# Kernel tuning notes

Hardware: AMD Instinct MI355X
Metric: run time of the kernel (lower is better)

The kernel has to match this reference:

```python
import jax, jax.numpy as jnp
import numpy as np

D = 512      # d_model
H = 8        # n_heads
DH = D // H  # d_head
WIN = 128    # window radius
FF = 4 * D   # ffn hidden
B, T = 4, 2048
EPS = 1e-5


def _ln(x, g, b):
    mu = jnp.mean(x, axis=-1, keepdims=True)
    var = jnp.mean((x - mu) ** 2, axis=-1, keepdims=True)
    return (x - mu) * jax.lax.rsqrt(var + EPS) * g + b


def _rope(x):
    # standard rotate-half RoPE over the full d_model dim (applied to ln(x)
    # before q/k/v projections, as in the source module)
    t, d = x.shape[-2], x.shape[-1]
    half = d // 2
    inv_freq = 1.0 / (10000.0 ** (jnp.arange(half, dtype=jnp.float32) / half))
    ang = jnp.arange(t, dtype=jnp.float32)[:, None] * inv_freq[None, :]  # (T, half)
    cos, sin = jnp.cos(ang), jnp.sin(ang)
    x1, x2 = x[..., :half], x[..., half:]
    return jnp.concatenate([x1 * cos - x2 * sin, x1 * sin + x2 * cos], axis=-1)


def setup_inputs() -> dict:
    key = jax.random.key(0)
    ks = jax.random.split(key, 16)
    s = 0.02
    inp = {
        "x": jax.random.normal(ks[0], (B, T, D), dtype=jnp.float32),
        "Wq": jax.random.normal(ks[1], (D, D), dtype=jnp.float32) * s,
        "bq": jnp.zeros((D,), jnp.float32),
        "Wk": jax.random.normal(ks[2], (D, D), dtype=jnp.float32) * s,
        "bk": jnp.zeros((D,), jnp.float32),
        "Wv": jax.random.normal(ks[3], (D, D), dtype=jnp.float32) * s,
        "bv": jnp.zeros((D,), jnp.float32),
        "Wo": jax.random.normal(ks[4], (D, D), dtype=jnp.float32) * s,
        "bo": jnp.zeros((D,), jnp.float32),
        "ln_g": jnp.ones((D,), jnp.float32),
        "ln_b": jnp.zeros((D,), jnp.float32),
        "ffln_g": jnp.ones((D,), jnp.float32),
        "ffln_b": jnp.zeros((D,), jnp.float32),
        "W1": jax.random.normal(ks[5], (D, FF), dtype=jnp.float32) * s,
        "b1": jnp.zeros((FF,), jnp.float32),
        "W2": jax.random.normal(ks[6], (FF, D), dtype=jnp.float32) * s,
        "b2": jnp.zeros((D,), jnp.float32),
    }
    return inp


def reference(x, Wq, bq, Wk, bk, Wv, bv, Wo, bo, ln_g, ln_b, ffln_g, ffln_b, W1, b1, W2, b2):
    b, t, d = x.shape
    h = _rope(_ln(x, ln_g, ln_b))
    q = (h @ Wq + bq).reshape(b, t, H, DH).transpose(0, 2, 1, 3)  # (B,H,T,DH)
    k = (h @ Wk + bk).reshape(b, t, H, DH).transpose(0, 2, 1, 3)
    v = (h @ Wv + bv).reshape(b, t, H, DH).transpose(0, 2, 1, 3)

    scores = jnp.einsum("bhqd,bhkd->bhqk", q, k) / jnp.sqrt(jnp.float32(DH))
    # Faithful to source local_mask semantics under torch SDPA bool-mask
    # convention (True = attend): attention is ALLOWED where |i-j| > window.
    idx = jnp.arange(t)
    allowed = jnp.abs(idx[:, None] - idx[None, :]) > WIN  # (T,T) bool
    scores = jnp.where(allowed, scores, -jnp.inf)
    attn = jax.nn.softmax(scores, axis=-1)
    o = jnp.einsum("bhqk,bhkd->bhqd", attn, v)
    o = o.transpose(0, 2, 1, 3).reshape(b, t, d)
    x = x + (o @ Wo + bo)

    # source applies self.ln AND the ff's internal LayerNorm back-to-back
    f = _ln(_ln(x, ln_g, ln_b), ffln_g, ffln_b)
    f = jax.nn.gelu(f @ W1 + b1, approximate=False) @ W2 + b2
    return x + f
```

## Files before the change

kernel.cpp:

```cpp
#include <hip/hip_runtime.h>
#include <cmath>

typedef __bf16 bf16x8 __attribute__((ext_vector_type(8)));
typedef float  f32x4  __attribute__((ext_vector_type(4)));
typedef float  f32x16 __attribute__((ext_vector_type(16)));

#define MFMA(a, b, c)   __builtin_amdgcn_mfma_f32_16x16x32_bf16((a), (b), (c), 0, 0, 0)
#define MFMA32(a, b, c) __builtin_amdgcn_mfma_f32_32x32x16_bf16((a), (b), (c), 0, 0, 0)

static __device__ __forceinline__ __bf16 f2bf(float f) {
  union { float f; unsigned u; } v; v.f = f;
  unsigned r = v.u + 0x7fffu + ((v.u >> 16) & 1u);
  union { unsigned short u; __bf16 b; } o; o.u = (unsigned short)(r >> 16);
  return o.b;
}
static __device__ __forceinline__ __bf16 f2bf_tr(float f) {
  union { float f; unsigned u; } v; v.f = f;
  union { unsigned short u; __bf16 b; } o; o.u = (unsigned short)(v.u >> 16);
  return o.b;
}

typedef const __attribute__((address_space(1))) void* gas_t;
typedef __attribute__((address_space(3))) void* las_t;
static __device__ __forceinline__ void load_lds16(const __bf16* g, __bf16* l) {
  __builtin_amdgcn_global_load_lds((gas_t)g, (las_t)l, 16, 0, 0);
}

__global__ __launch_bounds__(256) void k_transpose_all(
    const float* __restrict__ Wq, const float* __restrict__ Wk,
    const float* __restrict__ Wv, const float* __restrict__ Wo,
    const float* __restrict__ W1, const float* __restrict__ W2,
    __bf16* __restrict__ wqkv, __bf16* __restrict__ wo,
    __bf16* __restrict__ w1t, __bf16* __restrict__ w2t) {
  int idx = blockIdx.x * 256 + threadIdx.x;
  const float* src; __bf16* dst; int off, logK, N;
  if (idx < 1048576) {
    int which = idx >> 18; off = idx & 262143; logK = 9; N = 512;
    src = which == 0 ? Wq : which == 1 ? Wk : which == 2 ? Wv : Wo;
    dst = which < 3 ? wqkv + which * 262144 : wo;
  } else if (idx < 2097152) {
    off = idx - 1048576; logK = 9; N = 2048; src = W1; dst = w1t;
  } else {
    off = idx - 2097152; logK = 11; N = 512; src = W2; dst = w2t;
  }
  int n = off >> logK, k = off & ((1 << logK) - 1);
  dst[off] = f2bf(src[(size_t)k * N + n]);
}

__global__ __launch_bounds__(256) void k_ln_rope(const float* __restrict__ x,
                                                 const float* __restrict__ g,
                                                 const float* __restrict__ b,
                                                 __bf16* __restrict__ h) {
  int n = blockIdx.x, tid = threadIdx.x;
  const float* row = x + (size_t)n * 512;
  float v1 = row[tid], v2 = row[tid + 256];
  float s = v1 + v2, ss = v1 * v1 + v2 * v2;
  #pragma unroll
  for (int off = 1; off < 64; off <<= 1) { s += __shfl_xor(s, off, 64); ss += __shfl_xor(ss, off, 64); }
  __shared__ float red[2][4];
  if ((tid & 63) == 0) { red[0][tid >> 6] = s; red[1][tid >> 6] = ss; }
  __syncthreads();
  s  = red[0][0] + red[0][1] + red[0][2] + red[0][3];
  ss = red[1][0] + red[1][1] + red[1][2] + red[1][3];
  float mu = s * (1.f / 512.f);
  float var = ss * (1.f / 512.f) - mu * mu;
  float rs = rsqrtf(var + 1e-5f);
  float y1 = (v1 - mu) * rs * g[tid] + b[tid];
  float y2 = (v2 - mu) * rs * g[tid + 256] + b[tid + 256];
  int t = n & 2047;
  float inv = __expf(-(float)tid * 0.03597789207803197f);
  float ang = (float)t * inv;
  float sn, c;
  __sincosf(ang, &sn, &c);
  h[(size_t)n * 512 + tid]       = f2bf(y1 * c - y2 * sn);
  h[(size_t)n * 512 + tid + 256] = f2bf(y1 * sn + y2 * c);
}

template <int K>
static __device__ __forceinline__ void gemm128(const __bf16* __restrict__ A,
                                               const __bf16* __restrict__ Bt,
                                               f32x4 (&acc)[2][4]) {
  __shared__ __bf16 lA[128 * 64];
  __shared__ __bf16 lB[128 * 64];
  int bm = blockIdx.x & 63, bn = blockIdx.x >> 6;
  int tid = threadIdx.x, w = tid >> 6, lane = tid & 63;
  int l16 = lane & 15, quad = lane >> 4;
  int wr = (w & 3) * 32, wc = (w >> 2) * 64;
  int srow = w * 8 + (lane >> 3);
  int sg = (lane & 7) ^ (srow & 7);
  const __bf16* ga = A  + (size_t)(bm * 128 + srow) * K + sg * 8;
  const __bf16* gb = Bt + (size_t)(bn * 128 + srow) * K + sg * 8;
  __bf16* saw = lA + w * 512;
  __bf16* sbw = lB + w * 512;
  #pragma unroll
  for (int i = 0; i < 2; ++i)
    #pragma unroll
    for (int j = 0; j < 4; ++j) acc[i][j] = {0.f, 0.f, 0.f, 0.f};
  const size_t rstep = (size_t)64 * K;
  for (int k0 = 0; k0 < K; k0 += 64) {
    load_lds16(ga + k0,         saw);
    load_lds16(ga + k0 + rstep, saw + 4096);
    load_lds16(gb + k0,         sbw);
    load_lds16(gb + k0 + rstep, sbw + 4096);
    __syncthreads();
    #pragma unroll
    for (int kk = 0; kk < 2; ++kk) {
      int gg = kk * 4 + quad;
      bf16x8 af[2], bfr[4];
      #pragma unroll
      for (int i = 0; i < 2; ++i) {
        int row = wr + i * 16 + l16;
        __builtin_memcpy(&af[i], &lA[row * 64 + ((gg ^ (row & 7)) * 8)], 16);
      }
      #pragma unroll
      for (int j = 0; j < 4; ++j) {
        int row = wc + j * 16 + l16;
        __builtin_memcpy(&bfr[j], &lB[row * 64 + ((gg ^ (row & 7)) * 8)], 16);
      }
      #pragma unroll
      for (int i = 0; i < 2; ++i)
        #pragma unroll
        for (int j = 0; j < 4; ++j) acc[i][j] = MFMA(af[i], bfr[j], acc[i][j]);
    }
    __syncthreads();
  }
}

#define G128_EPILOG_IDX                                 \
  int bm = blockIdx.x & 63, bn = blockIdx.x >> 6;       \
  int lane = threadIdx.x & 63, w = threadIdx.x >> 6;    \
  int l16 = lane & 15, quad = lane >> 4;                \
  int wr = (w & 3) * 32, wc = (w >> 2) * 64;

__global__ __launch_bounds__(512) void k_gemm_qkv(const __bf16* __restrict__ A,
                                                  const __bf16* __restrict__ Bt,
                                                  const float* __restrict__ bq,
                                                  const float* __restrict__ bk,
                                                  const float* __restrict__ bv,
                                                  __bf16* __restrict__ qo,
                                                  __bf16* __restrict__ ko,
                                                  __bf16* __restrict__ vT) {
  f32x4 acc[2][4];
  gemm128<512>(A, Bt, acc);
  G128_EPILOG_IDX
  int proj = bn >> 2;
  const float* bias = proj == 0 ? bq : (proj == 1 ? bk : bv);
  float scale = proj == 0 ? 0.125f : 1.f;
  if (proj < 2) {
    __bf16* dst = proj == 0 ? qo : ko;
    #pragma unroll
    for (int i = 0; i < 2; ++i)
      #pragma unroll
      for (int j = 0; j < 4; ++j)
        #pragma unroll
        for (int r = 0; r < 4; ++r) {
          int c = (bn * 128 + wc + j * 16 + l16) & 511;
          int m = bm * 128 + wr + i * 16 + quad * 4 + r;
          int bI = m >> 11, t = m & 2047;
          int head = c >> 6, dh = c & 63;
          dst[(((size_t)bI * 8 + head) * 2048 + t) * 64 + dh] = f2bf((acc[i][j][r] + bias[c]) * scale);
        }
  } else {
    #pragma unroll
    for (int i = 0; i < 2; ++i)
      #pragma unroll
      for (int j = 0; j < 4; ++j)
        #pragma unroll
        for (int r = 0; r < 4; ++r) {
          int c = (bn * 128 + wc + j * 16 + l16) & 511;
          int m = bm * 128 + wr + i * 16 + quad * 4 + r;
          int bI = m >> 11, t = m & 2047;
          int head = c >> 6, dh = c & 63;
          vT[(((size_t)bI * 8 + head) * 64 + dh) * 2048 + t] = f2bf(acc[i][j][r] + bias[c]);
        }
  }
}

template <int K, typename EPI>
static __device__ __forceinline__ void gemm64sk(const __bf16* __restrict__ A,
                                                const __bf16* __restrict__ Bt,
                                                EPI epi) {
  __shared__ __align__(16) char smem[64 * 128 * 2 * 2];
  __bf16* lA = (__bf16*)smem;
  __bf16* lB = lA + 64 * 128;
  int bm = blockIdx.x & 127, bn = blockIdx.x >> 7;
  int tid = threadIdx.x, w = tid >> 6, lane = tid & 63;
  int l16 = lane & 15, quad = lane >> 4;
  int pos = w & 3, half = w >> 2;
  int wr = (pos >> 1) * 32, wc = (pos & 1) * 32;
  int srow = tid >> 4;
  int sg = (tid & 15) ^ (srow & 15);
  const __bf16* ga = A  + (size_t)(bm * 64 + srow) * K + sg * 8;
  const __bf16* gb = Bt + (size_t)(bn * 64 + srow) * K + sg * 8;
  __bf16* sa = lA + w * 512;
  __bf16* sb = lB + w * 512;
  f32x4 acc[2][2];
  #pragma unroll
  for (int i = 0; i < 2; ++i)
    #pragma unroll
    for (int j = 0; j < 2; ++j) acc[i][j] = {0.f, 0.f, 0.f, 0.f};
  const size_t rstep = (size_t)32 * K;
  for (int k0 = 0; k0 < K; k0 += 128) {
    load_lds16(ga + k0,         sa);
    load_lds16(ga + k0 + rstep, sa + 4096);
    load_lds16(gb + k0,         sb);
    load_lds16(gb + k0 + rstep, sb + 4096);
    __syncthreads();
    #pragma unroll
    for (int kk = 0; kk < 2; ++kk) {
      int gg = half * 8 + kk * 4 + quad;
      bf16x8 af[2], bfr[2];
      #pragma unroll
      for (int i = 0; i < 2; ++i) {
        int row = wr + i * 16 + l16;
        __builtin_memcpy(&af[i], &lA[row * 128 + ((gg ^ (row & 15)) * 8)], 16);
      }
      #pragma unroll
      for (int j = 0; j < 2; ++j) {
        int row = wc + j * 16 + l16;
        __builtin_memcpy(&bfr[j], &lB[row * 128 + ((gg ^ (row & 15)) * 8)], 16);
      }
      #pragma unroll
      for (int i = 0; i < 2; ++i)
        #pragma unroll
        for (int j = 0; j < 2; ++j) acc[i][j] = MFMA(af[i], bfr[j], acc[i][j]);
    }
    __syncthreads();
  }
  float (*cbuf)[64][17] = (float(*)[64][17])smem;
  if (half) {
    #pragma unroll
    for (int i = 0; i < 2; ++i)
      #pragma unroll
      for (int j = 0; j < 2; ++j)
        #pragma unroll
        for (int r = 0; r < 4; ++r) cbuf[pos][lane][(i * 2 + j) * 4 + r] = acc[i][j][r];
  }
  __syncthreads();
  if (!half) {
    #pragma unroll
    for (int i = 0; i < 2; ++i)
      #pragma unroll
      for (int j = 0; j < 2; ++j)
        #pragma unroll
        for (int r = 0; r < 4; ++r) {
          float v = acc[i][j][r] + cbuf[pos][lane][(i * 2 + j) * 4 + r];
          int m = bm * 64 + wr + i * 16 + quad * 4 + r;
          int n = bn * 64 + wc + j * 16 + l16;
          epi(m, n, v);
        }
  }
}

__global__ __launch_bounds__(512) void k_gemm_oproj(const __bf16* __restrict__ A,
                                                    const __bf16* __restrict__ Bt,
                                                    const float* __restrict__ bo,
                                                    const float* __restrict__ xin,
                                                    float* __restrict__ x2) {
  gemm64sk<512>(A, Bt, [&](int m, int n, float v) {
    size_t idx = (size_t)m * 512 + n;
    x2[idx] = xin[idx] + v + bo[n];
  });
}

__global__ __launch_bounds__(512) void k_gemm_ffn2(const __bf16* __restrict__ A,
                                                   const __bf16* __restrict__ Bt,
                                                   const float* __restrict__ b2,
                                                   const float* __restrict__ x2,
                                                   float* __restrict__ out) {
  gemm64sk<2048>(A, Bt, [&](int m, int n, float v) {
    size_t idx = (size_t)m * 512 + n;
    out[idx] = x2[idx] + v + b2[n];
  });
}

__global__ __launch_bounds__(512) void k_attn(const __bf16* __restrict__ q,
                                              const __bf16* __restrict__ k,
                                              const __bf16* __restrict__ vT,
                                              __bf16* __restrict__ o) {
  __shared__ __align__(16) __bf16 Kt[64 * 64];
  __shared__ __align__(16) __bf16 Vt[64 * 64];
  __shared__ __align__(16) __bf16 P[8][32][40];
  __shared__ float cbuf[4][64][17];
  int bh = blockIdx.x >> 4, qblk = blockIdx.x & 15;
  int tid = threadIdx.x, w = tid >> 6, lane = tid & 63;
  int l32 = lane & 31, h32 = lane >> 5;
  int qw = w & 3, half = w >> 2, hoff = half * 32;
  int qB = qblk * 128;
  int q0 = qB + qw * 32;
  const __bf16* qb = q + (size_t)bh * 2048 * 64;
  const __bf16* kb = k + (size_t)bh * 2048 * 64;
  const __bf16* vb = vT + (size_t)bh * 64 * 2048;
  bf16x8 aq[4];
  #pragma unroll
  for (int i = 0; i < 4; ++i)
    aq[i] = *(const bf16x8*)(qb + (size_t)(q0 + l32) * 64 + i * 16 + h32 * 8);
  f32x16 on0 = {0,0,0,0,0,0,0,0,0,0,0,0,0,0,0,0};
  f32x16 on1 = {0,0,0,0,0,0,0,0,0,0,0,0,0,0,0,0};
  float lsum[16];
  #pragma unroll
  for (int i = 0; i < 16; ++i) lsum[i] = 0.f;
  int srow = w * 8 + (lane >> 3);
  int sg = (lane & 7) ^ (srow & 7);
  const __bf16* gk = kb + (size_t)srow * 64 + sg * 8;
  const __bf16* gv = vb + (size_t)srow * 2048 + sg * 8;
  __bf16* skw = Kt + w * 512;
  __bf16* svw = Vt + w * 512;

  for (int it = 0; it < 32; ++it) {
    int kt64 = it * 64;
    if ((unsigned)(kt64 - qB) <= 64u) continue;
    load_lds16(gk + (size_t)kt64 * 64, skw);
    load_lds16(gv + kt64, svw);
    __syncthreads();
    int myk0 = kt64 + hoff;
    bool skip = (q0 + 31 - myk0 <= 128) && (myk0 + 31 - q0 <= 128);
    if (!skip) {
      bool need_mask = !((myk0 >= q0 + 160) || (myk0 <= q0 - 160));
      f32x16 sc = {0,0,0,0,0,0,0,0,0,0,0,0,0,0,0,0};
      int krow = hoff + l32;
      #pragma unroll
      for (int i = 0; i < 4; ++i) {
        int gg = i * 2 + h32;
        bf16x8 bk;
        __builtin_memcpy(&bk, &Kt[krow * 64 + ((gg ^ (l32 & 7)) * 8)], 16);
        sc = MFMA32(aq[i], bk, sc);
      }
      #pragma unroll
      for (int reg = 0; reg < 16; ++reg) {
        int row = (reg & 3) + 8 * (reg >> 2) + 4 * h32;
        float p = __expf(sc[reg]);
        if (need_mask) {
          int qi = q0 + row, kj = myk0 + l32;
          if ((unsigned)(qi - kj + 128) <= 256u) p = 0.f;
        }
        P[w][row][l32] = f2bf_tr(p);
        lsum[reg] += p;
      }
      bf16x8 ap0, ap1;
      __builtin_memcpy(&ap0, &P[w][l32][h32 * 8], 16);
      __builtin_memcpy(&ap1, &P[w][l32][16 + h32 * 8], 16);
      #pragma unroll
      for (int kk = 0; kk < 2; ++kk) {
        bf16x8 ap = kk ? ap1 : ap0;
        int gg = half * 4 + kk * 2 + h32;
        bf16x8 bv0, bv1;
        __builtin_memcpy(&bv0, &Vt[l32 * 64 + ((gg ^ (l32 & 7)) * 8)], 16);
        __builtin_memcpy(&bv1, &Vt[(32 + l32) * 64 + ((gg ^ (l32 & 7)) * 8)], 16);
        on0 = MFMA32(ap, bv0, on0);
        on1 = MFMA32(ap, bv1, on1);
      }
    }
    __syncthreads();
  }
  if (half) {
    for (int i = 0; i < 16; ++i) cbuf[qw][lane][i] = on0[i];
  }
  __syncthreads();
  if (!half) {
    for (int i = 0; i < 16; ++i) on0[i] += cbuf[qw][lane][i];
  }
  __syncthreads();
  if (half) {
    for (int i = 0; i < 16; ++i) cbuf[qw][lane][i] = on1[i];
  }
  __syncthreads();
  if (!half) {
    for (int i = 0; i < 16; ++i) on1[i] += cbuf[qw][lane][i];
  }
  __syncthreads();
  if (half) {
    for (int i = 0; i < 16; ++i) cbuf[qw][lane][i] = lsum[i];
  }
  __syncthreads();
  if (!half) {
    #pragma unroll
    for (int i = 0; i < 16; ++i) {
      float s = lsum[i] + cbuf[qw][lane][i];
      #pragma unroll
      for (int off = 1; off < 32; off <<= 1) s += __shfl_xor(s, off, 64);
      lsum[i] = 1.f / s;
    }
    int bI = bh >> 3, head = bh & 7;
    #pragma unroll
    for (int reg = 0; reg < 16; ++reg) {
      int row = (reg & 3) + 8 * (reg >> 2) + 4 * h32;
      size_t base = ((size_t)(bI * 2048 + q0 + row)) * 512 + head * 64;
      o[base + l32]      = f2bf(on0[reg] * lsum[reg]);
      o[base + 32 + l32] = f2bf(on1[reg] * lsum[reg]);
    }
  }
}

__global__ __launch_bounds__(256) void k_ln_ln(const float* __restrict__ x2,
                                               const float* __restrict__ g1v,
                                               const float* __restrict__ b1v,
                                               const float* __restrict__ g2v,
                                               const float* __restrict__ b2v,
                                               __bf16* __restrict__ fout) {
  int n = blockIdx.x, tid = threadIdx.x;
  const float* row = x2 + (size_t)n * 512;
  float v1 = row[tid], v2 = row[tid + 256];
  __shared__ float red[2][4];
  float s = v1 + v2, ss = v1 * v1 + v2 * v2;
  #pragma unroll
  for (int off = 1; off < 64; off <<= 1) { s += __shfl_xor(s, off, 64); ss += __shfl_xor(ss, off, 64); }
  if ((tid & 63) == 0) { red[0][tid >> 6] = s; red[1][tid >> 6] = ss; }
  __syncthreads();
  s  = red[0][0] + red[0][1] + red[0][2] + red[0][3];
  ss = red[1][0] + red[1][1] + red[1][2] + red[1][3];
  float mu = s * (1.f / 512.f), var = ss * (1.f / 512.f) - mu * mu;
  float rs = rsqrtf(var + 1e-5f);
  float y1 = (v1 - mu) * rs * g1v[tid] + b1v[tid];
  float y2 = (v2 - mu) * rs * g1v[tid + 256] + b1v[tid + 256];
  __syncthreads();
  s = y1 + y2; ss = y1 * y1 + y2 * y2;
  #pragma unroll
  for (int off = 1; off < 64; off <<= 1) { s += __shfl_xor(s, off, 64); ss += __shfl_xor(ss, off, 64); }
  if ((tid & 63) == 0) { red[0][tid >> 6] = s; red[1][tid >> 6] = ss; }
  __syncthreads();
  s  = red[0][0] + red[0][1] + red[0][2] + red[0][3];
  ss = red[1][0] + red[1][1] + red[1][2] + red[1][3];
  float mu2 = s * (1.f / 512.f), var2 = ss * (1.f / 512.f) - mu2 * mu2;
  float rs2 = rsqrtf(var2 + 1e-5f);
  fout[(size_t)n * 512 + tid]       = f2bf((y1 - mu2) * rs2 * g2v[tid] + b2v[tid]);
  fout[(size_t)n * 512 + tid + 256] = f2bf((y2 - mu2) * rs2 * g2v[tid + 256] + b2v[tid + 256]);
}

__global__ __launch_bounds__(512) void k_gemm_ffn1(const __bf16* __restrict__ A,
                                                   const __bf16* __restrict__ Bt,
                                                   const float* __restrict__ b1,
                                                   __bf16* __restrict__ g1) {
  f32x4 acc[2][4];
  gemm128<512>(A, Bt, acc);
  G128_EPILOG_IDX
  #pragma unroll
  for (int i = 0; i < 2; ++i)
    #pragma unroll
    for (int j = 0; j < 4; ++j)
      #pragma unroll
      for (int r = 0; r < 4; ++r) {
        int n = bn * 128 + wc + j * 16 + l16;
        int m = bm * 128 + wr + i * 16 + quad * 4 + r;
        float t = acc[i][j][r] + b1[n];
        float ge = 0.5f * t * (1.f + erff(t * 0.7071067811865475f));
        g1[(size_t)m * 2048 + n] = f2bf(ge);
      }
}

extern "C" void kernel_launch(void* const* d_in, const int* in_sizes, int n_in,
                              void* d_out, int out_size, void* d_ws, size_t ws_size,
                              hipStream_t stream) {
  (void)in_sizes; (void)n_in; (void)out_size; (void)ws_size;
  const float* x   = (const float*)d_in[0];
  const float* Wq  = (const float*)d_in[1];
  const float* bq  = (const float*)d_in[2];
  const float* Wk  = (const float*)d_in[3];
  const float* bk  = (const float*)d_in[4];
  const float* Wv  = (const float*)d_in[5];
  const float* bv  = (const float*)d_in[6];
  const float* Wo  = (const float*)d_in[7];
  const float* bo  = (const float*)d_in[8];
  const float* lng = (const float*)d_in[9];
  const float* lnb = (const float*)d_in[10];
  const float* ffg = (const float*)d_in[11];
  const float* ffb = (const float*)d_in[12];
  const float* W1  = (const float*)d_in[13];
  const float* b1  = (const float*)d_in[14];
  const float* W2  = (const float*)d_in[15];
  const float* b2  = (const float*)d_in[16];
  float* out = (float*)d_out;

  char* ws = (char*)d_ws;
  __bf16* h    = (__bf16*)(ws);
  __bf16* qb   = (__bf16*)(ws + (size_t)8 * 1024 * 1024);
  __bf16* kb   = (__bf16*)(ws + (size_t)16 * 1024 * 1024);
  __bf16* vT   = (__bf16*)(ws + (size_t)24 * 1024 * 1024);
  float*  x2   = (float*)(ws + (size_t)32 * 1024 * 1024);
  __bf16* fb   = (__bf16*)(ws + (size_t)48 * 1024 * 1024);
  __bf16* wqkv = (__bf16*)(ws + (size_t)56 * 1024 * 1024);
  __bf16* wo   = wqkv + 3 * 512 * 512;
  __bf16* w1t  = wo + 512 * 512;
  __bf16* w2t  = w1t + 512 * 2048;
  __bf16* g1   = (__bf16*)(ws);

  k_transpose_all<<<12288, 256, 0, stream>>>(Wq, Wk, Wv, Wo, W1, W2, wqkv, wo, w1t, w2t);
  k_ln_rope<<<8192, 256, 0, stream>>>(x, lng, lnb, h);
  k_gemm_qkv<<<64 * 12, 512, 0, stream>>>(h, wqkv, bq, bk, bv, qb, kb, vT);
  k_attn<<<32 * 16, 512, 0, stream>>>(qb, kb, vT, h);
  k_gemm_oproj<<<128 * 8, 512, 0, stream>>>(h, wo, bo, x, x2);
  k_ln_ln<<<8192, 256, 0, stream>>>(x2, lng, lnb, ffg, ffb, fb);
  k_gemm_ffn1<<<64 * 16, 512, 0, stream>>>(fb, w1t, b1, g1);
  k_gemm_ffn2<<<128 * 8, 512, 0, stream>>>(g1, w2t, b2, x2, out);
}
```

Measured before the change: 277.1 us.

## Keep attention probabilities in registers via transposed MFMA and merge prep kernels

The attention kernel now computes S^T by swapping the MFMA operands, so each lane holds one query's scores. The probabilities are packed to bf16 in registers and exchanged across half-waves with shuffles, replacing the P shared-memory round trip. This also reduces the row-sum to a single scalar per lane and writes output as packed 8-byte stores. Separately, the weight-transpose and LN+RoPE kernels are merged into one launch to save a kernel boundary. The costs are extra shuffle and select instructions, and a risk of layout mistakes in the operand swap.

```diff
diff --git a/kernel.cpp b/kernel.cpp
--- a/kernel.cpp
+++ b/kernel.cpp
@@ -4,20 +4,24 @@
 typedef __bf16 bf16x8 __attribute__((ext_vector_type(8)));
 typedef float  f32x4  __attribute__((ext_vector_type(4)));
 typedef float  f32x16 __attribute__((ext_vector_type(16)));
+typedef int    i32x4  __attribute__((ext_vector_type(4)));
 
 #define MFMA(a, b, c)   __builtin_amdgcn_mfma_f32_16x16x32_bf16((a), (b), (c), 0, 0, 0)
 #define MFMA32(a, b, c) __builtin_amdgcn_mfma_f32_32x32x16_bf16((a), (b), (c), 0, 0, 0)
 
+static __device__ __forceinline__ unsigned fbits(float f) {
+  union { float f; unsigned u; } v; v.f = f; return v.u;
+}
 static __device__ __forceinline__ __bf16 f2bf(float f) {
-  union { float f; unsigned u; } v; v.f = f;
-  unsigned r = v.u + 0x7fffu + ((v.u >> 16) & 1u);
+  unsigned u = fbits(f);
+  unsigned r = u + 0x7fffu + ((u >> 16) & 1u);
   union { unsigned short u; __bf16 b; } o; o.u = (unsigned short)(r >> 16);
   return o.b;
 }
-static __device__ __forceinline__ __bf16 f2bf_tr(float f) {
-  union { float f; unsigned u; } v; v.f = f;
-  union { unsigned short u; __bf16 b; } o; o.u = (unsigned short)(v.u >> 16);
-  return o.b;
+static __device__ __forceinline__ unsigned pack2rn(float a, float b) {
+  unsigned ua = fbits(a); ua = ua + 0x7fffu + ((ua >> 16) & 1u);
+  unsigned ub = fbits(b); ub = ub + 0x7fffu + ((ub >> 16) & 1u);
+  return __builtin_amdgcn_perm(ub, ua, 0x07060302);
 }
 
 typedef const __attribute__((address_space(1))) void* gas_t;
@@ -26,32 +30,31 @@
   __builtin_amdgcn_global_load_lds((gas_t)g, (las_t)l, 16, 0, 0);
 }
 
-__global__ __launch_bounds__(256) void k_transpose_all(
+__global__ __launch_bounds__(256) void k_pre(
     const float* __restrict__ Wq, const float* __restrict__ Wk,
     const float* __restrict__ Wv, const float* __restrict__ Wo,
     const float* __restrict__ W1, const float* __restrict__ W2,
     __bf16* __restrict__ wqkv, __bf16* __restrict__ wo,
-    __bf16* __restrict__ w1t, __bf16* __restrict__ w2t) {
-  int idx = blockIdx.x * 256 + threadIdx.x;
-  const float* src; __bf16* dst; int off, logK, N;
-  if (idx < 1048576) {
-    int which = idx >> 18; off = idx & 262143; logK = 9; N = 512;
-    src = which == 0 ? Wq : which == 1 ? Wk : which == 2 ? Wv : Wo;
-    dst = which < 3 ? wqkv + which * 262144 : wo;
-  } else if (idx < 2097152) {
-    off = idx - 1048576; logK = 9; N = 2048; src = W1; dst = w1t;
-  } else {
-    off = idx - 2097152; logK = 11; N = 512; src = W2; dst = w2t;
-  }
-  int n = off >> logK, k = off & ((1 << logK) - 1);
-  dst[off] = f2bf(src[(size_t)k * N + n]);
-}
-
-__global__ __launch_bounds__(256) void k_ln_rope(const float* __restrict__ x,
-                                                 const float* __restrict__ g,
-                                                 const float* __restrict__ b,
-                                                 __bf16* __restrict__ h) {
-  int n = blockIdx.x, tid = threadIdx.x;
+    __bf16* __restrict__ w1t, __bf16* __restrict__ w2t,
+    const float* __restrict__ x, const float* __restrict__ g,
+    const float* __restrict__ b, __bf16* __restrict__ h) {
+  if (blockIdx.x < 12288) {
+    int idx = blockIdx.x * 256 + threadIdx.x;
+    const float* src; __bf16* dst; int off, logK, N;
+    if (idx < 1048576) {
+      int which = idx >> 18; off = idx & 262143; logK = 9; N = 512;
+      src = which == 0 ? Wq : which == 1 ? Wk : which == 2 ? Wv : Wo;
+      dst = which < 3 ? wqkv + which * 262144 : wo;
+    } else if (idx < 2097152) {
+      off = idx - 1048576; logK = 9; N = 2048; src = W1; dst = w1t;
+    } else {
+      off = idx - 2097152; logK = 11; N = 512; src = W2; dst = w2t;
+    }
+    int n = off >> logK, k = off & ((1 << logK) - 1);
+    dst[off] = f2bf(src[(size_t)k * N + n]);
+    return;
+  }
+  int n = blockIdx.x - 12288, tid = threadIdx.x;
   const float* row = x + (size_t)n * 512;
   float v1 = row[tid], v2 = row[tid + 256];
   float s = v1 + v2, ss = v1 * v1 + v2 * v2;
@@ -280,7 +283,6 @@
                                               __bf16* __restrict__ o) {
   __shared__ __align__(16) __bf16 Kt[64 * 64];
   __shared__ __align__(16) __bf16 Vt[64 * 64];
-  __shared__ __align__(16) __bf16 P[8][32][40];
   __shared__ float cbuf[4][64][17];
   int bh = blockIdx.x >> 4, qblk = blockIdx.x & 15;
   int tid = threadIdx.x, w = tid >> 6, lane = tid & 63;
@@ -288,18 +290,17 @@
   int qw = w & 3, half = w >> 2, hoff = half * 32;
   int qB = qblk * 128;
   int q0 = qB + qw * 32;
+  int qglob = q0 + l32;
   const __bf16* qb = q + (size_t)bh * 2048 * 64;
   const __bf16* kb = k + (size_t)bh * 2048 * 64;
   const __bf16* vb = vT + (size_t)bh * 64 * 2048;
   bf16x8 aq[4];
   #pragma unroll
   for (int i = 0; i < 4; ++i)
-    aq[i] = *(const bf16x8*)(qb + (size_t)(q0 + l32) * 64 + i * 16 + h32 * 8);
+    aq[i] = *(const bf16x8*)(qb + (size_t)qglob * 64 + i * 16 + h32 * 8);
   f32x16 on0 = {0,0,0,0,0,0,0,0,0,0,0,0,0,0,0,0};
   f32x16 on1 = {0,0,0,0,0,0,0,0,0,0,0,0,0,0,0,0};
-  float lsum[16];
-  #pragma unroll
-  for (int i = 0; i < 16; ++i) lsum[i] = 0.f;
+  float lsum = 0.f;
   int srow = w * 8 + (lane >> 3);
   int sg = (lane & 7) ^ (srow & 7);
   const __bf16* gk = kb + (size_t)srow * 64 + sg * 8;
@@ -323,32 +324,42 @@
       for (int i = 0; i < 4; ++i) {
         int gg = i * 2 + h32;
         bf16x8 bk;
-        __builtin_memcpy(&bk, &Kt[krow * 64 + ((gg ^ (l32 & 7)) * 8)], 16);
-        sc = MFMA32(aq[i], bk, sc);
-      }
-      #pragma unroll
-      for (int reg = 0; reg < 16; ++reg) {
-        int row = (reg & 3) + 8 * (reg >> 2) + 4 * h32;
-        float p = __expf(sc[reg]);
+        __builtin_memcpy(&bk, &Kt[krow * 64 + ((gg ^ (krow & 7)) * 8)], 16);
+        sc = MFMA32(bk, aq[i], sc);
+      }
+      unsigned pk[8];
+      #pragma unroll
+      for (int g2 = 0; g2 < 8; ++g2) {
+        int r0 = 2 * g2;
+        float p0 = __expf(sc[r0]);
+        float p1 = __expf(sc[r0 + 1]);
         if (need_mask) {
-          int qi = q0 + row, kj = myk0 + l32;
-          if ((unsigned)(qi - kj + 128) <= 256u) p = 0.f;
+          int k0l = (r0 & 3) + 8 * (r0 >> 2) + 4 * h32;
+          if ((unsigned)(qglob - (myk0 + k0l) + 128) <= 256u) p0 = 0.f;
+          if ((unsigned)(qglob - (myk0 + k0l + 1) + 128) <= 256u) p1 = 0.f;
         }
-        P[w][row][l32] = f2bf_tr(p);
-        lsum[reg] += p;
-      }
-      bf16x8 ap0, ap1;
-      __builtin_memcpy(&ap0, &P[w][l32][h32 * 8], 16);
-      __builtin_memcpy(&ap1, &P[w][l32][16 + h32 * 8], 16);
+        lsum += p0 + p1;
+        pk[g2] = __builtin_amdgcn_perm(fbits(p1), fbits(p0), 0x07060302);
+      }
+      unsigned ex[8];
+      #pragma unroll
+      for (int g2 = 0; g2 < 8; ++g2) ex[g2] = (unsigned)__shfl_xor((int)pk[g2], 32);
       #pragma unroll
       for (int kk = 0; kk < 2; ++kk) {
-        bf16x8 ap = kk ? ap1 : ap0;
+        int o4 = kk * 4;
+        i32x4 fi;
+        fi.x = (int)(h32 ? ex[o4 + 2] : pk[o4 + 0]);
+        fi.y = (int)(h32 ? ex[o4 + 3] : pk[o4 + 1]);
+        fi.z = (int)(h32 ? pk[o4 + 2] : ex[o4 + 0]);
+        fi.w = (int)(h32 ? pk[o4 + 3] : ex[o4 + 1]);
+        bf16x8 pf;
+        __builtin_memcpy(&pf, &fi, 16);
         int gg = half * 4 + kk * 2 + h32;
         bf16x8 bv0, bv1;
         __builtin_memcpy(&bv0, &Vt[l32 * 64 + ((gg ^ (l32 & 7)) * 8)], 16);
         __builtin_memcpy(&bv1, &Vt[(32 + l32) * 64 + ((gg ^ (l32 & 7)) * 8)], 16);
-        on0 = MFMA32(ap, bv0, on0);
-        on1 = MFMA32(ap, bv1, on1);
+        on0 = MFMA32(bv0, pf, on0);
+        on1 = MFMA32(bv1, pf, on1);
       }
     }
     __syncthreads();
@@ -370,24 +381,25 @@
   }
   __syncthreads();
   if (half) {
-    for (int i = 0; i < 16; ++i) cbuf[qw][lane][i] = lsum[i];
+    cbuf[qw][lane][0] = lsum;
   }
   __syncthreads();
   if (!half) {
-    #pragma unroll
-    for (int i = 0; i < 16; ++i) {
-      float s = lsum[i] + cbuf[qw][lane][i];
-      #pragma unroll
-      for (int off = 1; off < 32; off <<= 1) s += __shfl_xor(s, off, 64);
-      lsum[i] = 1.f / s;
-    }
+    float s = lsum + cbuf[qw][lane][0];
+    s += __shfl_xor(s, 32);
+    float rl = 1.f / s;
     int bI = bh >> 3, head = bh & 7;
-    #pragma unroll
-    for (int reg = 0; reg < 16; ++reg) {
-      int row = (reg & 3) + 8 * (reg >> 2) + 4 * h32;
-      size_t base = ((size_t)(bI * 2048 + q0 + row)) * 512 + head * 64;
-      o[base + l32]      = f2bf(on0[reg] * lsum[reg]);
-      o[base + 32 + l32] = f2bf(on1[reg] * lsum[reg]);
+    __bf16* obase = o + ((size_t)(bI * 2048 + qglob)) * 512 + head * 64 + 4 * h32;
+    #pragma unroll
+    for (int g2 = 0; g2 < 4; ++g2) {
+      int r0 = 4 * g2;
+      int2 v0, v1;
+      v0.x = (int)pack2rn(on0[r0] * rl, on0[r0 + 1] * rl);
+      v0.y = (int)pack2rn(on0[r0 + 2] * rl, on0[r0 + 3] * rl);
+      v1.x = (int)pack2rn(on1[r0] * rl, on1[r0 + 1] * rl);
+      v1.y = (int)pack2rn(on1[r0 + 2] * rl, on1[r0 + 3] * rl);
+      *(int2*)(obase + 8 * g2) = v0;
+      *(int2*)(obase + 32 + 8 * g2) = v1;
     }
   }
 }
@@ -484,8 +496,8 @@
   __bf16* w2t  = w1t + 512 * 2048;
   __bf16* g1   = (__bf16*)(ws);
 
-  k_transpose_all<<<12288, 256, 0, stream>>>(Wq, Wk, Wv, Wo, W1, W2, wqkv, wo, w1t, w2t);
-  k_ln_rope<<<8192, 256, 0, stream>>>(x, lng, lnb, h);
+  k_pre<<<12288 + 8192, 256, 0, stream>>>(Wq, Wk, Wv, Wo, W1, W2, wqkv, wo, w1t, w2t,
+                                          x, lng, lnb, h);
   k_gemm_qkv<<<64 * 12, 512, 0, stream>>>(h, wqkv, bq, bk, bv, qb, kb, vT);
   k_attn<<<32 * 16, 512, 0, stream>>>(qb, kb, vT, h);
   k_gemm_oproj<<<128 * 8, 512, 0, stream>>>(h, wo, bo, x, x2);
```

Result: no change. 277.0 us (-0.1%).
